# Kernel optimization log

Measured on AMD Instinct MI355X. Metric: run time of the kernel, lower is better.

## Reference

```python
import jax, jax.numpy as jnp
import numpy as np

EPS = 1e-12  # torch F.normalize eps

def _l2norm(v, axis):
    return v / jnp.maximum(jnp.linalg.norm(v, axis=axis, keepdims=True), EPS)

def setup_inputs() -> dict:
    key = jax.random.key(0)
    k1, k2, k3, k4 = jax.random.split(key, 4)
    n, K, d, H, W = 32, 64, 256, 64, 64
    x = jax.random.normal(k1, (n, d, H, W), dtype=jnp.float32)
    conv_w = jax.random.normal(k2, (K, d), dtype=jnp.float32) * 0.05
    conv_b = jax.random.normal(k3, (K,), dtype=jnp.float32) * 0.05
    centroids = jax.random.uniform(k4, (K, d), dtype=jnp.float32)
    return {"x": x, "conv_w": conv_w, "conv_b": conv_b, "centroids": centroids}

def reference(x, conv_w, conv_b, centroids):
    n, c, H, W = x.shape
    K = centroids.shape[0]
    # input L2 normalization over channel dim
    x = _l2norm(x, axis=1)
    x_flat = x.reshape(n, c, H * W)                      # [n, c, S]
    # 1x1 conv == matmul over channels, then softmax over clusters
    logits = jnp.einsum('kc,ncs->nks', conv_w, x_flat) + conv_b[None, :, None]
    a = jax.nn.softmax(logits, axis=1)                   # [n, K, S]
    # vlad[n,k,c] = sum_s a[n,k,s] * (x[n,c,s] - cent[k,c])
    #            = (a @ x^T) - cent * sum_s a   (GEMM reformulation)
    vlad = jnp.einsum('nks,ncs->nkc', a, x_flat)
    vlad = vlad - a.sum(axis=2)[:, :, None] * centroids[None, :, :]
    # intra-normalize per cluster, flatten, global L2 normalize
    vlad = _l2norm(vlad, axis=2)
    vlad = vlad.reshape(n, K * c)
    vlad = _l2norm(vlad, axis=1)
    return vlad
```

## Files before the change

### kernel.cpp

```cpp
#include <hip/hip_runtime.h>
#include <math.h>

#define NIMG 32
#define CDIM 256
#define KCL  64
#define SPIX 4096

__global__ __launch_bounds__(256) void k_wt(const float* __restrict__ w, float* __restrict__ wT) {
    int g = blockIdx.x * 256 + threadIdx.x;
    if (g < KCL * CDIM) {
        int k = g / CDIM, c = g % CDIM;
        wT[c * KCL + k] = w[g];
    }
}

#define WFMA32() \
    acc[0]=fmaf(w0_.x,xv,acc[0]);   acc[1]=fmaf(w0_.y,xv,acc[1]); \
    acc[2]=fmaf(w0_.z,xv,acc[2]);   acc[3]=fmaf(w0_.w,xv,acc[3]); \
    acc[4]=fmaf(w1_.x,xv,acc[4]);   acc[5]=fmaf(w1_.y,xv,acc[5]); \
    acc[6]=fmaf(w1_.z,xv,acc[6]);   acc[7]=fmaf(w1_.w,xv,acc[7]); \
    acc[8]=fmaf(w2_.x,xv,acc[8]);   acc[9]=fmaf(w2_.y,xv,acc[9]); \
    acc[10]=fmaf(w2_.z,xv,acc[10]); acc[11]=fmaf(w2_.w,xv,acc[11]); \
    acc[12]=fmaf(w3_.x,xv,acc[12]); acc[13]=fmaf(w3_.y,xv,acc[13]); \
    acc[14]=fmaf(w3_.z,xv,acc[14]); acc[15]=fmaf(w3_.w,xv,acc[15]); \
    acc[16]=fmaf(w4_.x,xv,acc[16]); acc[17]=fmaf(w4_.y,xv,acc[17]); \
    acc[18]=fmaf(w4_.z,xv,acc[18]); acc[19]=fmaf(w4_.w,xv,acc[19]); \
    acc[20]=fmaf(w5_.x,xv,acc[20]); acc[21]=fmaf(w5_.y,xv,acc[21]); \
    acc[22]=fmaf(w5_.z,xv,acc[22]); acc[23]=fmaf(w5_.w,xv,acc[23]); \
    acc[24]=fmaf(w6_.x,xv,acc[24]); acc[25]=fmaf(w6_.y,xv,acc[25]); \
    acc[26]=fmaf(w6_.z,xv,acc[26]); acc[27]=fmaf(w6_.w,xv,acc[27]); \
    acc[28]=fmaf(w7_.x,xv,acc[28]); acc[29]=fmaf(w7_.y,xv,acc[29]); \
    acc[30]=fmaf(w7_.z,xv,acc[30]); acc[31]=fmaf(w7_.w,xv,acc[31]);

__global__ __launch_bounds__(512, 4) void k_logits(const float* __restrict__ x,
                                                   const float* __restrict__ wT,
                                                   const float* __restrict__ b,
                                                   float* __restrict__ aT,
                                                   float* __restrict__ inv_norm,
                                                   float* __restrict__ asum_part) {
    int blk = blockIdx.x;
    int n = blk >> 4, g = blk & 15;
    int s0 = g * 256;
    int tid = threadIdx.x;
    int wv = tid >> 6, l = tid & 63;
    int sl = tid & 255;
    int khu = __builtin_amdgcn_readfirstlane(tid >> 8);

    __shared__ float xs[32 * 256];
    __shared__ float4 red4[8 * 64];
    __shared__ float redf[512];
    __shared__ float invs[256];

    float acc[32];
    #pragma unroll
    for (int i = 0; i < 32; i++) acc[i] = 0.f;
    float4 sq = {0.f, 0.f, 0.f, 0.f};

    int cst = tid >> 6;
    int p4 = (tid & 63) * 4;

    for (int t = 0; t < 8; t++) {
        if (t) __syncthreads();
        #pragma unroll
        for (int i = 0; i < 4; i++) {
            int c = cst + 8 * i;
            float4 xq = *(const float4*)(x + ((size_t)(n * CDIM + t * 32 + c)) * SPIX + s0 + p4);
            sq.x = fmaf(xq.x, xq.x, sq.x);
            sq.y = fmaf(xq.y, xq.y, sq.y);
            sq.z = fmaf(xq.z, xq.z, sq.z);
            sq.w = fmaf(xq.w, xq.w, sq.w);
            *(float4*)(xs + c * 256 + p4) = xq;
        }
        __syncthreads();
        const float* wrow = wT + (size_t)(t * 32) * KCL + khu * 32;
        #pragma unroll 8
        for (int cc = 0; cc < 32; cc++) {
            float xv = xs[cc * 256 + sl];
            const float4* wp = (const float4*)(wrow + (size_t)cc * KCL);
            float4 w0_=wp[0], w1_=wp[1], w2_=wp[2], w3_=wp[3];
            float4 w4_=wp[4], w5_=wp[5], w6_=wp[6], w7_=wp[7];
            WFMA32()
        }
    }

    red4[wv * 64 + l] = sq;
    __syncthreads();
    float4 ssq = red4[l];
    #pragma unroll
    for (int i = 1; i < 8; i++) {
        float4 t4 = red4[i * 64 + l];
        ssq.x += t4.x; ssq.y += t4.y; ssq.z += t4.z; ssq.w += t4.w;
    }
    if (wv == 0) {
        float4 invn;
        invn.x = 1.f / fmaxf(sqrtf(ssq.x), 1e-12f);
        invn.y = 1.f / fmaxf(sqrtf(ssq.y), 1e-12f);
        invn.z = 1.f / fmaxf(sqrtf(ssq.z), 1e-12f);
        invn.w = 1.f / fmaxf(sqrtf(ssq.w), 1e-12f);
        *(float4*)(invs + 4 * l) = invn;
        *(float4*)(inv_norm + (size_t)n * SPIX + s0 + 4 * l) = invn;
    }
    __syncthreads();
    float invp = invs[sl];

    const float* bb = b + khu * 32;
    #pragma unroll
    for (int i = 0; i < 32; i++) acc[i] = fmaf(acc[i], invp, bb[i]);

    float m = acc[0];
    #pragma unroll
    for (int i = 1; i < 32; i++) m = fmaxf(m, acc[i]);
    redf[tid] = m;
    __syncthreads();
    m = fmaxf(redf[sl], redf[256 + sl]);
    float ssum = 0.f;
    #pragma unroll
    for (int i = 0; i < 32; i++) { float e = __expf(acc[i] - m); acc[i] = e; ssum += e; }
    __syncthreads();
    redf[tid] = ssum;
    __syncthreads();
    float r = 1.0f / (redf[sl] + redf[256 + sl]);
    #pragma unroll
    for (int i = 0; i < 32; i++) acc[i] *= r;

    float4* ap = (float4*)(aT + ((size_t)(n * SPIX + s0 + sl)) * KCL + khu * 32);
    #pragma unroll
    for (int j = 0; j < 8; j++) {
        float4 v = {acc[4*j+0], acc[4*j+1], acc[4*j+2], acc[4*j+3]};
        ap[j] = v;
    }

    #pragma unroll
    for (int i = 0; i < 32; i++) {
        float v = acc[i];
        #pragma unroll
        for (int off = 32; off > 0; off >>= 1) v += __shfl_xor(v, off, 64);
        if (l == 0) asum_part[(blk * 8 + wv) * 32 + i] = v;
    }
}

__global__ __launch_bounds__(512, 4) void k_vlad(const float* __restrict__ x,
                                                 const float* __restrict__ inv_norm,
                                                 const float* __restrict__ aT,
                                                 float* __restrict__ vlad_part) {
    int blk = blockIdx.x;
    int n = blk >> 4, g = blk & 15;
    int tid = threadIdx.x;
    int kh = __builtin_amdgcn_readfirstlane(tid >> 8);
    int c = tid & 255;

    __shared__ float xt[256 * 33];

    float acc[32];
    #pragma unroll
    for (int i = 0; i < 32; i++) acc[i] = 0.f;

    int sl = tid & 31;
    int cr = tid >> 5;

    for (int t = 0; t < 8; t++) {
        int s0 = g * 256 + t * 32;
        float invp = inv_norm[n * SPIX + s0 + sl];
        __syncthreads();
        #pragma unroll
        for (int i = 0; i < 16; i++) {
            int cc = cr + i * 16;
            xt[cc * 33 + sl] = x[((size_t)n * CDIM + cc) * SPIX + s0 + sl] * invp;
        }
        __syncthreads();

        const float* ab = aT + ((size_t)(n * SPIX + s0)) * KCL + kh * 32;
        for (int ss = 0; ss < 32; ss++) {
            float xn = xt[c * 33 + ss];
            const float4* ap = (const float4*)(ab + ss * 64);
            #pragma unroll
            for (int q = 0; q < 8; q++) {
                float4 a4 = ap[q];
                acc[4*q+0] = fmaf(a4.x, xn, acc[4*q+0]);
                acc[4*q+1] = fmaf(a4.y, xn, acc[4*q+1]);
                acc[4*q+2] = fmaf(a4.z, xn, acc[4*q+2]);
                acc[4*q+3] = fmaf(a4.w, xn, acc[4*q+3]);
            }
        }
    }
    float* vp = vlad_part + ((size_t)blk * KCL + kh * 32) * CDIM + c;
    #pragma unroll
    for (int i = 0; i < 32; i++) vp[(size_t)i * CDIM] = acc[i];
}

__global__ __launch_bounds__(256) void k_combine(const float* __restrict__ vlad_part,
                                                 const float* __restrict__ asum_part,
                                                 const float* __restrict__ cent,
                                                 float* __restrict__ out,
                                                 float* __restrict__ rs) {
    int blk = blockIdx.x;
    int n = blk >> 6, k = blk & 63;
    int c = threadIdx.x;
    float v = 0.f;
    for (int j = 0; j < 16; j++)
        v += vlad_part[(((size_t)(n * 16 + j)) * KCL + k) * CDIM + c];
    float as = 0.f;
    int kh = k >> 5, kj = k & 31;
    for (int j = 0; j < 16; j++)
        for (int q = 0; q < 4; q++)
            as += asum_part[(((n * 16 + j) * 8) + kh * 4 + q) * 32 + kj];
    v = fmaf(-as, cent[k * CDIM + c], v);

    float t = v * v;
    #pragma unroll
    for (int off = 32; off > 0; off >>= 1) t += __shfl_xor(t, off, 64);
    __shared__ float w4[4];
    int lane = threadIdx.x & 63, wid = threadIdx.x >> 6;
    if (lane == 0) w4[wid] = t;
    __syncthreads();
    float ss = w4[0] + w4[1] + w4[2] + w4[3];
    float inv = 1.0f / fmaxf(sqrtf(ss), 1e-12f);
    out[(size_t)blk * CDIM + c] = v * inv;
    if (threadIdx.x == 0) rs[blk] = ss * inv * inv;
}

__global__ __launch_bounds__(256) void k_gnorm(const float* __restrict__ rs,
                                               float* __restrict__ out) {
    int n = blockIdx.x >> 3, j = blockIdx.x & 7;
    float ss = 0.f;
    for (int k = 0; k < KCL; k++) ss += rs[n * KCL + k];
    float g = 1.0f / fmaxf(sqrtf(ss), 1e-12f);
    size_t base = (size_t)n * (KCL * CDIM) + j * 2048 + threadIdx.x;
    for (int i = 0; i < 8; i++) out[base + i * 256] *= g;
}

extern "C" void kernel_launch(void* const* d_in, const int* in_sizes, int n_in,
                              void* d_out, int out_size, void* d_ws, size_t ws_size,
                              hipStream_t stream) {
    const float* x    = (const float*)d_in[0];
    const float* w    = (const float*)d_in[1];
    const float* b    = (const float*)d_in[2];
    const float* cent = (const float*)d_in[3];
    float* out = (float*)d_out;

    float* ws = (float*)d_ws;
    float* wT        = ws;
    float* inv_norm  = wT + 16384;
    float* aT        = inv_norm + 131072;
    float* vlad_part = aT + 8388608;
    float* asum_part = vlad_part + 8388608;
    float* rs        = asum_part + 131072;

    k_wt<<<64, 256, 0, stream>>>(w, wT);
    k_logits<<<512, 512, 0, stream>>>(x, wT, b, aT, inv_norm, asum_part);
    k_vlad<<<512, 512, 0, stream>>>(x, inv_norm, aT, vlad_part);
    k_combine<<<2048, 256, 0, stream>>>(vlad_part, asum_part, cent, out, rs);
    k_gnorm<<<256, 256, 0, stream>>>(rs, out);
}
```

Measured before the change: 185.3 us.

## Remap logits kernel to lane-per-cluster with LDS weights and shuffle softmax

Restructures k_logits so each lane owns one cluster and each wave owns 32 pixels. The weights are staged in LDS per 32-channel chunk, and x is read from global with wave-uniform (broadcast) addresses instead of being staged in shared memory. Softmax becomes cross-lane shuffle reductions per pixel, and the cluster-sum partials are reduced in the block to one value per cluster, which simplifies the combine kernel. The aim is to drop the x staging and the two-half softmax exchange through shared memory. In exchange, x is now read twice (once for the norm pass, once for the matmul) and each pixel needs many shuffles.

```diff
diff --git a/kernel.cpp b/kernel.cpp
--- a/kernel.cpp
+++ b/kernel.cpp
@@ -13,24 +13,6 @@
         wT[c * KCL + k] = w[g];
     }
 }
-
-#define WFMA32() \
-    acc[0]=fmaf(w0_.x,xv,acc[0]);   acc[1]=fmaf(w0_.y,xv,acc[1]); \
-    acc[2]=fmaf(w0_.z,xv,acc[2]);   acc[3]=fmaf(w0_.w,xv,acc[3]); \
-    acc[4]=fmaf(w1_.x,xv,acc[4]);   acc[5]=fmaf(w1_.y,xv,acc[5]); \
-    acc[6]=fmaf(w1_.z,xv,acc[6]);   acc[7]=fmaf(w1_.w,xv,acc[7]); \
-    acc[8]=fmaf(w2_.x,xv,acc[8]);   acc[9]=fmaf(w2_.y,xv,acc[9]); \
-    acc[10]=fmaf(w2_.z,xv,acc[10]); acc[11]=fmaf(w2_.w,xv,acc[11]); \
-    acc[12]=fmaf(w3_.x,xv,acc[12]); acc[13]=fmaf(w3_.y,xv,acc[13]); \
-    acc[14]=fmaf(w3_.z,xv,acc[14]); acc[15]=fmaf(w3_.w,xv,acc[15]); \
-    acc[16]=fmaf(w4_.x,xv,acc[16]); acc[17]=fmaf(w4_.y,xv,acc[17]); \
-    acc[18]=fmaf(w4_.z,xv,acc[18]); acc[19]=fmaf(w4_.w,xv,acc[19]); \
-    acc[20]=fmaf(w5_.x,xv,acc[20]); acc[21]=fmaf(w5_.y,xv,acc[21]); \
-    acc[22]=fmaf(w5_.z,xv,acc[22]); acc[23]=fmaf(w5_.w,xv,acc[23]); \
-    acc[24]=fmaf(w6_.x,xv,acc[24]); acc[25]=fmaf(w6_.y,xv,acc[25]); \
-    acc[26]=fmaf(w6_.z,xv,acc[26]); acc[27]=fmaf(w6_.w,xv,acc[27]); \
-    acc[28]=fmaf(w7_.x,xv,acc[28]); acc[29]=fmaf(w7_.y,xv,acc[29]); \
-    acc[30]=fmaf(w7_.z,xv,acc[30]); acc[31]=fmaf(w7_.w,xv,acc[31]);
 
 __global__ __launch_bounds__(512, 4) void k_logits(const float* __restrict__ x,
                                                    const float* __restrict__ wT,
@@ -43,55 +25,35 @@
     int s0 = g * 256;
     int tid = threadIdx.x;
     int wv = tid >> 6, l = tid & 63;
-    int sl = tid & 255;
-    int khu = __builtin_amdgcn_readfirstlane(tid >> 8);
-
-    __shared__ float xs[32 * 256];
+    int wvu = __builtin_amdgcn_readfirstlane(wv);
+
+    __shared__ float wlds[32 * 64];
     __shared__ float4 red4[8 * 64];
-    __shared__ float redf[512];
     __shared__ float invs[256];
-
-    float acc[32];
-    #pragma unroll
-    for (int i = 0; i < 32; i++) acc[i] = 0.f;
+    __shared__ float reda[8 * 64];
+
     float4 sq = {0.f, 0.f, 0.f, 0.f};
-
-    int cst = tid >> 6;
-    int p4 = (tid & 63) * 4;
-
+    int p4 = l * 4;
     for (int t = 0; t < 8; t++) {
-        if (t) __syncthreads();
         #pragma unroll
         for (int i = 0; i < 4; i++) {
-            int c = cst + 8 * i;
-            float4 xq = *(const float4*)(x + ((size_t)(n * CDIM + t * 32 + c)) * SPIX + s0 + p4);
+            int c = t * 32 + wvu + 8 * i;
+            float4 xq = *(const float4*)(x + ((size_t)(n * CDIM + c)) * SPIX + s0 + p4);
             sq.x = fmaf(xq.x, xq.x, sq.x);
             sq.y = fmaf(xq.y, xq.y, sq.y);
             sq.z = fmaf(xq.z, xq.z, sq.z);
             sq.w = fmaf(xq.w, xq.w, sq.w);
-            *(float4*)(xs + c * 256 + p4) = xq;
-        }
-        __syncthreads();
-        const float* wrow = wT + (size_t)(t * 32) * KCL + khu * 32;
-        #pragma unroll 8
-        for (int cc = 0; cc < 32; cc++) {
-            float xv = xs[cc * 256 + sl];
-            const float4* wp = (const float4*)(wrow + (size_t)cc * KCL);
-            float4 w0_=wp[0], w1_=wp[1], w2_=wp[2], w3_=wp[3];
-            float4 w4_=wp[4], w5_=wp[5], w6_=wp[6], w7_=wp[7];
-            WFMA32()
-        }
-    }
-
+        }
+    }
     red4[wv * 64 + l] = sq;
     __syncthreads();
-    float4 ssq = red4[l];
-    #pragma unroll
-    for (int i = 1; i < 8; i++) {
-        float4 t4 = red4[i * 64 + l];
-        ssq.x += t4.x; ssq.y += t4.y; ssq.z += t4.z; ssq.w += t4.w;
-    }
     if (wv == 0) {
+        float4 ssq = red4[l];
+        #pragma unroll
+        for (int i = 1; i < 8; i++) {
+            float4 t4 = red4[i * 64 + l];
+            ssq.x += t4.x; ssq.y += t4.y; ssq.z += t4.z; ssq.w += t4.w;
+        }
         float4 invn;
         invn.x = 1.f / fmaxf(sqrtf(ssq.x), 1e-12f);
         invn.y = 1.f / fmaxf(sqrtf(ssq.y), 1e-12f);
@@ -100,42 +62,56 @@
         *(float4*)(invs + 4 * l) = invn;
         *(float4*)(inv_norm + (size_t)n * SPIX + s0 + 4 * l) = invn;
     }
+
+    float acc[32];
+    #pragma unroll
+    for (int i = 0; i < 32; i++) acc[i] = 0.f;
+
+    int pbase = 32 * wvu;
+    const float* xb = x + ((size_t)n * CDIM) * SPIX + s0 + pbase;
+
+    for (int t = 0; t < 8; t++) {
+        __syncthreads();
+        ((float4*)wlds)[tid] = ((const float4*)(wT + (size_t)(t * 32) * KCL))[tid];
+        __syncthreads();
+        for (int cc = 0; cc < 32; cc++) {
+            float wl = wlds[cc * 64 + l];
+            const float4* xp = (const float4*)(xb + (size_t)(t * 32 + cc) * SPIX);
+            #pragma unroll
+            for (int q = 0; q < 8; q++) {
+                float4 x4 = xp[q];
+                acc[4*q+0] = fmaf(x4.x, wl, acc[4*q+0]);
+                acc[4*q+1] = fmaf(x4.y, wl, acc[4*q+1]);
+                acc[4*q+2] = fmaf(x4.z, wl, acc[4*q+2]);
+                acc[4*q+3] = fmaf(x4.w, wl, acc[4*q+3]);
+            }
+        }
+    }
+
+    float bl = b[l];
+    float asum_l = 0.f;
+    float* aout = aT + ((size_t)(n * SPIX + s0 + pbase)) * KCL + l;
+    #pragma unroll
+    for (int p = 0; p < 32; p++) {
+        float lg = fmaf(acc[p], invs[pbase + p], bl);
+        float m = lg;
+        #pragma unroll
+        for (int off = 32; off > 0; off >>= 1) m = fmaxf(m, __shfl_xor(m, off, 64));
+        float e = __expf(lg - m);
+        float ss = e;
+        #pragma unroll
+        for (int off = 32; off > 0; off >>= 1) ss += __shfl_xor(ss, off, 64);
+        float a = e * (1.f / ss);
+        aout[(size_t)p * KCL] = a;
+        asum_l += a;
+    }
+    reda[wv * 64 + l] = asum_l;
     __syncthreads();
-    float invp = invs[sl];
-
-    const float* bb = b + khu * 32;
-    #pragma unroll
-    for (int i = 0; i < 32; i++) acc[i] = fmaf(acc[i], invp, bb[i]);
-
-    float m = acc[0];
-    #pragma unroll
-    for (int i = 1; i < 32; i++) m = fmaxf(m, acc[i]);
-    redf[tid] = m;
-    __syncthreads();
-    m = fmaxf(redf[sl], redf[256 + sl]);
-    float ssum = 0.f;
-    #pragma unroll
-    for (int i = 0; i < 32; i++) { float e = __expf(acc[i] - m); acc[i] = e; ssum += e; }
-    __syncthreads();
-    redf[tid] = ssum;
-    __syncthreads();
-    float r = 1.0f / (redf[sl] + redf[256 + sl]);
-    #pragma unroll
-    for (int i = 0; i < 32; i++) acc[i] *= r;
-
-    float4* ap = (float4*)(aT + ((size_t)(n * SPIX + s0 + sl)) * KCL + khu * 32);
-    #pragma unroll
-    for (int j = 0; j < 8; j++) {
-        float4 v = {acc[4*j+0], acc[4*j+1], acc[4*j+2], acc[4*j+3]};
-        ap[j] = v;
-    }
-
-    #pragma unroll
-    for (int i = 0; i < 32; i++) {
-        float v = acc[i];
-        #pragma unroll
-        for (int off = 32; off > 0; off >>= 1) v += __shfl_xor(v, off, 64);
-        if (l == 0) asum_part[(blk * 8 + wv) * 32 + i] = v;
+    if (wv == 0) {
+        float t = reda[l];
+        #pragma unroll
+        for (int i = 1; i < 8; i++) t += reda[i * 64 + l];
+        asum_part[blk * KCL + l] = t;
     }
 }
 
@@ -200,10 +176,8 @@
     for (int j = 0; j < 16; j++)
         v += vlad_part[(((size_t)(n * 16 + j)) * KCL + k) * CDIM + c];
     float as = 0.f;
-    int kh = k >> 5, kj = k & 31;
     for (int j = 0; j < 16; j++)
-        for (int q = 0; q < 4; q++)
-            as += asum_part[(((n * 16 + j) * 8) + kh * 4 + q) * 32 + kj];
+        as += asum_part[(n * 16 + j) * KCL + k];
     v = fmaf(-as, cent[k * CDIM + c], v);
 
     float t = v * v;
@@ -244,7 +218,7 @@
     float* aT        = inv_norm + 131072;
     float* vlad_part = aT + 8388608;
     float* asum_part = vlad_part + 8388608;
-    float* rs        = asum_part + 131072;
+    float* rs        = asum_part + 32768;
 
     k_wt<<<64, 256, 0, stream>>>(w, wT);
     k_logits<<<512, 512, 0, stream>>>(x, wT, b, aT, inv_norm, asum_part);
```

Measured after the change: 356.4 us. 1.92x slower.
